# Kernel optimization log

Measured on AMD Instinct MI355X. Metric: run time of the kernel, lower is better.

## Reference

```python
import jax, jax.numpy as jnp
import numpy as np

B = 262144
INPUT_DIM = 512
HID = 64
NUM_BASE = 2
NUM_CLASSES = 2


def setup_inputs() -> dict:
    key = jax.random.key(0)
    ks = jax.random.split(key, 10)
    probs = jax.random.uniform(ks[0], (B, NUM_BASE, NUM_CLASSES), dtype=jnp.float32)
    fuzzy_features = jax.random.normal(ks[1], (B, INPUT_DIM), dtype=jnp.float32)
    s1 = 1.0 / np.sqrt(INPUT_DIM)
    s2 = 1.0 / np.sqrt(HID)
    # m1: Linear(input_dim,64) -> ReLU -> Linear(64, num_base*num_classes)
    W1 = jax.random.uniform(ks[2], (INPUT_DIM, HID), jnp.float32, -s1, s1)
    b1 = jax.random.uniform(ks[3], (HID,), jnp.float32, -s1, s1)
    W2 = jax.random.uniform(ks[4], (HID, NUM_BASE * NUM_CLASSES), jnp.float32, -s2, s2)
    b2 = jax.random.uniform(ks[5], (NUM_BASE * NUM_CLASSES,), jnp.float32, -s2, s2)
    # m2: Linear(input_dim,64) -> ReLU -> Linear(64, num_classes)
    W3 = jax.random.uniform(ks[6], (INPUT_DIM, HID), jnp.float32, -s1, s1)
    b3 = jax.random.uniform(ks[7], (HID,), jnp.float32, -s1, s1)
    W4 = jax.random.uniform(ks[8], (HID, NUM_CLASSES), jnp.float32, -s2, s2)
    b4 = jax.random.uniform(ks[9], (NUM_CLASSES,), jnp.float32, -s2, s2)
    return {"probs": probs, "fuzzy_features": fuzzy_features,
            "W1": W1, "b1": b1, "W2": W2, "b2": b2,
            "W3": W3, "b3": b3, "W4": W4, "b4": b4}


def _forward(probs, x, W1, b1, W2, b2, W3, b3, W4, b4):
    # FuzzyMeasureLearner
    h1 = jax.nn.relu(x @ W1 + b1)                       # [B, 64]
    single = jax.nn.sigmoid((h1 @ W2 + b2).reshape(-1, NUM_BASE, NUM_CLASSES))
    h2 = jax.nn.relu(x @ W3 + b3)                       # [B, 64]
    inc = jax.nn.sigmoid(h2 @ W4 + b4)                  # [B, 2]
    # Vectorized Choquet integral (binary, 2 sources)
    p0 = probs[:, 0, :]                                 # [B, 2]
    p1 = probs[:, 1, :]
    mu1 = single[:, 0, :]
    mu2 = single[:, 1, :]
    mu12 = jnp.minimum(jnp.maximum(mu1, mu2) + inc, 1.0)
    res = jnp.where(p0 <= p1,
                    p0 * mu1 + (p1 - p0) * mu12,
                    p1 * mu2 + (p0 - p1) * mu12)        # [B, 2]
    return jax.nn.softmax(res, axis=1)


def reference(probs, fuzzy_features, W1, b1, W2, b2, W3, b3, W4, b4):
    return _forward(probs, fuzzy_features, W1, b1, W2, b2, W3, b3, W4, b4)
```

## Files before the change

kernel.cpp:

```cpp
#include <hip/hip_runtime.h>
#include <hip/hip_bf16.h>

typedef short s16x8 __attribute__((ext_vector_type(8)));
typedef unsigned u32x4 __attribute__((ext_vector_type(4)));
typedef float f32x4 __attribute__((ext_vector_type(4)));
typedef float f32x2 __attribute__((ext_vector_type(2)));

static __device__ __forceinline__ short f2bf(float f) {
    unsigned u = __builtin_bit_cast(unsigned, f);
    unsigned r = (u + 0x7fffu + ((u >> 16) & 1u)) >> 16;
    return (short)r;
}

static __device__ __forceinline__ unsigned pk2bf(float a, float b) {
    __hip_bfloat162 h = __float22bfloat162_rn(make_float2(a, b));
    unsigned r;
    __builtin_memcpy(&r, &h, sizeof(r));
    return r;
}

__global__ void prep_weights(const float* __restrict__ W1,
                             const float* __restrict__ W3,
                             short* __restrict__ bws) {
    int tid = blockIdx.x * blockDim.x + threadIdx.x;
    int j  = tid & 7;
    int l  = (tid >> 3) & 63;
    int nt = (tid >> 9) & 7;
    int kk = tid >> 12;
    int k = kk * 32 + ((l >> 4) << 3) + j;
    int n = nt * 16 + (l & 15);
    float v = (n < 64) ? W1[k * 64 + n] : W3[k * 64 + (n - 64)];
    bws[tid] = f2bf(v);
}

__global__ __launch_bounds__(256, 2)
void mf2_main(const float* __restrict__ probs, const float* __restrict__ x,
              const short* __restrict__ bws,
              const float* __restrict__ b1, const float* __restrict__ W2,
              const float* __restrict__ b2, const float* __restrict__ b3,
              const float* __restrict__ W4, const float* __restrict__ b4,
              float* __restrict__ out)
{
    const int lane = threadIdx.x & 63;
    const int wv   = threadIdx.x >> 6;
    const int g    = lane >> 4;
    const int m    = lane & 15;
    const long rowBase = (long)blockIdx.x * 256 + wv * 64;

    f32x4 acc[4][8];
    #pragma unroll
    for (int t = 0; t < 4; ++t)
        #pragma unroll
        for (int nt = 0; nt < 8; ++nt)
            acc[t][nt] = (f32x4){0.f, 0.f, 0.f, 0.f};

    const float* xp = x + (rowBase + m) * 512 + g * 8;
    const s16x8* bp = (const s16x8*)bws + lane;

    f32x4 ra[4][2];
    #pragma unroll
    for (int t = 0; t < 4; ++t) {
        const float* p = xp + t * (16 * 512);
        ra[t][0] = __builtin_nontemporal_load((const f32x4*)p);
        ra[t][1] = __builtin_nontemporal_load((const f32x4*)(p + 4));
    }

    #pragma unroll 2
    for (int kk = 0; kk < 16; ++kk) {
        s16x8 b[8];
        #pragma unroll
        for (int nt = 0; nt < 8; ++nt) b[nt] = bp[kk * 512 + nt * 64];

        s16x8 a[4];
        #pragma unroll
        for (int t = 0; t < 4; ++t) {
            u32x4 pa;
            pa[0] = pk2bf(ra[t][0][0], ra[t][0][1]);
            pa[1] = pk2bf(ra[t][0][2], ra[t][0][3]);
            pa[2] = pk2bf(ra[t][1][0], ra[t][1][1]);
            pa[3] = pk2bf(ra[t][1][2], ra[t][1][3]);
            a[t] = __builtin_bit_cast(s16x8, pa);
        }

        if (kk < 15) {
            #pragma unroll
            for (int t = 0; t < 4; ++t) {
                const float* p = xp + t * (16 * 512) + (kk + 1) * 32;
                ra[t][0] = __builtin_nontemporal_load((const f32x4*)p);
                ra[t][1] = __builtin_nontemporal_load((const f32x4*)(p + 4));
            }
        }

        #pragma unroll
        for (int nt = 0; nt < 8; ++nt)
            #pragma unroll
            for (int t = 0; t < 4; ++t)
                acc[t][nt] = __builtin_amdgcn_mfma_f32_16x16x32_bf16(a[t], b[nt], acc[t][nt], 0, 0, 0);
    }

    float w2r[4][4];
    float w4r[4][2];
    float biasr[8];
    #pragma unroll
    for (int nt = 0; nt < 4; ++nt) {
        const int col = m + 16 * nt;
        f32x4 w2v = *(const f32x4*)(W2 + col * 4);
        #pragma unroll
        for (int c = 0; c < 4; ++c) w2r[nt][c] = w2v[c];
        f32x2 w4v = *(const f32x2*)(W4 + col * 2);
        w4r[nt][0] = w4v[0]; w4r[nt][1] = w4v[1];
    }
    #pragma unroll
    for (int nt = 0; nt < 8; ++nt) {
        const int col = m + 16 * nt;
        biasr[nt] = (col < 64) ? b1[col] : b3[col - 64];
    }
    float b2v[4], b4v[2];
    #pragma unroll
    for (int c = 0; c < 4; ++c) b2v[c] = b2[c];
    #pragma unroll
    for (int c = 0; c < 2; ++c) b4v[c] = b4[c];

    float own[6] = {0.f, 0.f, 0.f, 0.f, 0.f, 0.f};
    #pragma unroll
    for (int t = 0; t < 4; ++t) {
        #pragma unroll
        for (int r = 0; r < 4; ++r) {
            float v[6] = {0.f, 0.f, 0.f, 0.f, 0.f, 0.f};
            #pragma unroll
            for (int nt = 0; nt < 4; ++nt) {
                float h = fmaxf(acc[t][nt][r] + biasr[nt], 0.f);
                v[0] += h * w2r[nt][0];
                v[1] += h * w2r[nt][1];
                v[2] += h * w2r[nt][2];
                v[3] += h * w2r[nt][3];
            }
            #pragma unroll
            for (int j = 0; j < 4; ++j) {
                float h = fmaxf(acc[t][4 + j][r] + biasr[4 + j], 0.f);
                v[4] += h * w4r[j][0];
                v[5] += h * w4r[j][1];
            }
            #pragma unroll
            for (int msk = 1; msk <= 8; msk <<= 1) {
                #pragma unroll
                for (int c = 0; c < 6; ++c) v[c] += __shfl_xor(v[c], msk, 64);
            }
            if (m == t * 4 + r) {
                #pragma unroll
                for (int c = 0; c < 6; ++c) own[c] = v[c];
            }
        }
    }

    {
        const int t = m >> 2, r = m & 3;
        const long row = rowBase + t * 16 + g * 4 + r;
        f32x4 pr = *(const f32x4*)(probs + row * 4);
        float mu1[2], mu2[2], icv[2];
        #pragma unroll
        for (int c = 0; c < 2; ++c) {
            mu1[c] = 1.0f / (1.0f + __expf(-(own[c]     + b2v[c])));
            mu2[c] = 1.0f / (1.0f + __expf(-(own[2 + c] + b2v[2 + c])));
            icv[c] = 1.0f / (1.0f + __expf(-(own[4 + c] + b4v[c])));
        }
        float res[2];
        #pragma unroll
        for (int c = 0; c < 2; ++c) {
            float p0 = pr[c], p1 = pr[2 + c];
            float m12 = fminf(fmaxf(mu1[c], mu2[c]) + icv[c], 1.0f);
            res[c] = (p0 <= p1) ? (p0 * mu1[c] + (p1 - p0) * m12)
                                : (p1 * mu2[c] + (p0 - p1) * m12);
        }
        float d01 = res[0] - res[1];
        f32x2 o;
        o[0] = 1.0f / (1.0f + __expf(-d01));
        o[1] = 1.0f / (1.0f + __expf(d01));
        *(f32x2*)(out + row * 2) = o;
    }
}

extern "C" void kernel_launch(void* const* d_in, const int* in_sizes, int n_in,
                              void* d_out, int out_size, void* d_ws, size_t ws_size,
                              hipStream_t stream)
{
    const float* probs = (const float*)d_in[0];
    const float* x     = (const float*)d_in[1];
    const float* W1    = (const float*)d_in[2];
    const float* b1    = (const float*)d_in[3];
    const float* W2    = (const float*)d_in[4];
    const float* b2    = (const float*)d_in[5];
    const float* W3    = (const float*)d_in[6];
    const float* b3    = (const float*)d_in[7];
    const float* W4    = (const float*)d_in[8];
    const float* b4    = (const float*)d_in[9];
    float* out = (float*)d_out;
    short* bws = (short*)d_ws;

    hipLaunchKernelGGL(prep_weights, dim3(256), dim3(256), 0, stream, W1, W3, bws);
    hipLaunchKernelGGL(mf2_main, dim3(1024), dim3(256), 0, stream,
                       probs, x, bws, b1, W2, b2, b3, W4, b4, out);
}
```

Measured before the change: 146.4 us.

## Load 128 contiguous bytes per lane with K-permuted weights and smaller wave tiles

The packed weight layout is permuted in K so that each lane can read 32 contiguous floats (128 bytes) of x per row chunk instead of 8 scattered floats, with the MFMA k-ordering matched to the permutation. Each wave now handles 32 rows instead of 64, and the grid is doubled to 2048 blocks. The aim is wider, more coalesced global reads and more waves in flight to hide memory latency on this bandwidth-bound GEMV-like stage. The cost is more register pressure from 16 prefetched vectors per lane, and B-fragment reloads that are reused over only 2 row tiles instead of 4.

```diff
diff --git a/kernel.cpp b/kernel.cpp
--- a/kernel.cpp
+++ b/kernel.cpp
@@ -27,7 +27,8 @@
     int l  = (tid >> 3) & 63;
     int nt = (tid >> 9) & 7;
     int kk = tid >> 12;
-    int k = kk * 32 + ((l >> 4) << 3) + j;
+    int g  = l >> 4;
+    int k = ((kk >> 2) << 7) + (g << 5) + ((kk & 3) << 3) + j;
     int n = nt * 16 + (l & 15);
     float v = (n < 64) ? W1[k * 64 + n] : W3[k * 64 + (n - 64)];
     bws[tid] = f2bf(v);
@@ -45,57 +46,61 @@
     const int wv   = threadIdx.x >> 6;
     const int g    = lane >> 4;
     const int m    = lane & 15;
-    const long rowBase = (long)blockIdx.x * 256 + wv * 64;
-
-    f32x4 acc[4][8];
-    #pragma unroll
-    for (int t = 0; t < 4; ++t)
+    const long rowBase = (long)blockIdx.x * 128 + wv * 32;
+
+    f32x4 acc[2][8];
+    #pragma unroll
+    for (int t = 0; t < 2; ++t)
         #pragma unroll
         for (int nt = 0; nt < 8; ++nt)
             acc[t][nt] = (f32x4){0.f, 0.f, 0.f, 0.f};
 
-    const float* xp = x + (rowBase + m) * 512 + g * 8;
+    const float* xp = x + (rowBase + m) * 512 + g * 32;
     const s16x8* bp = (const s16x8*)bws + lane;
 
-    f32x4 ra[4][2];
-    #pragma unroll
-    for (int t = 0; t < 4; ++t) {
-        const float* p = xp + t * (16 * 512);
-        ra[t][0] = __builtin_nontemporal_load((const f32x4*)p);
-        ra[t][1] = __builtin_nontemporal_load((const f32x4*)(p + 4));
-    }
-
-    #pragma unroll 2
-    for (int kk = 0; kk < 16; ++kk) {
-        s16x8 b[8];
-        #pragma unroll
-        for (int nt = 0; nt < 8; ++nt) b[nt] = bp[kk * 512 + nt * 64];
-
-        s16x8 a[4];
-        #pragma unroll
-        for (int t = 0; t < 4; ++t) {
-            u32x4 pa;
-            pa[0] = pk2bf(ra[t][0][0], ra[t][0][1]);
-            pa[1] = pk2bf(ra[t][0][2], ra[t][0][3]);
-            pa[2] = pk2bf(ra[t][1][0], ra[t][1][1]);
-            pa[3] = pk2bf(ra[t][1][2], ra[t][1][3]);
-            a[t] = __builtin_bit_cast(s16x8, pa);
-        }
-
-        if (kk < 15) {
-            #pragma unroll
-            for (int t = 0; t < 4; ++t) {
-                const float* p = xp + t * (16 * 512) + (kk + 1) * 32;
-                ra[t][0] = __builtin_nontemporal_load((const f32x4*)p);
-                ra[t][1] = __builtin_nontemporal_load((const f32x4*)(p + 4));
-            }
-        }
-
-        #pragma unroll
-        for (int nt = 0; nt < 8; ++nt)
-            #pragma unroll
-            for (int t = 0; t < 4; ++t)
-                acc[t][nt] = __builtin_amdgcn_mfma_f32_16x16x32_bf16(a[t], b[nt], acc[t][nt], 0, 0, 0);
+    f32x4 ra[2][8];
+    #pragma unroll
+    for (int t = 0; t < 2; ++t)
+        #pragma unroll
+        for (int q = 0; q < 8; ++q)
+            ra[t][q] = __builtin_nontemporal_load((const f32x4*)(xp + t * (16 * 512)) + q);
+
+    #pragma unroll
+    for (int c = 0; c < 4; ++c) {
+        s16x8 a[2][4];
+        #pragma unroll
+        for (int t = 0; t < 2; ++t)
+            #pragma unroll
+            for (int s = 0; s < 4; ++s) {
+                u32x4 pa;
+                pa[0] = pk2bf(ra[t][2 * s][0],     ra[t][2 * s][1]);
+                pa[1] = pk2bf(ra[t][2 * s][2],     ra[t][2 * s][3]);
+                pa[2] = pk2bf(ra[t][2 * s + 1][0], ra[t][2 * s + 1][1]);
+                pa[3] = pk2bf(ra[t][2 * s + 1][2], ra[t][2 * s + 1][3]);
+                a[t][s] = __builtin_bit_cast(s16x8, pa);
+            }
+
+        if (c < 3) {
+            #pragma unroll
+            for (int t = 0; t < 2; ++t)
+                #pragma unroll
+                for (int q = 0; q < 8; ++q)
+                    ra[t][q] = __builtin_nontemporal_load(
+                        (const f32x4*)(xp + t * (16 * 512) + (c + 1) * 128) + q);
+        }
+
+        #pragma unroll
+        for (int s = 0; s < 4; ++s) {
+            const int kk = c * 4 + s;
+            s16x8 b[8];
+            #pragma unroll
+            for (int nt = 0; nt < 8; ++nt) b[nt] = bp[kk * 512 + nt * 64];
+            #pragma unroll
+            for (int nt = 0; nt < 8; ++nt)
+                #pragma unroll
+                for (int t = 0; t < 2; ++t)
+                    acc[t][nt] = __builtin_amdgcn_mfma_f32_16x16x32_bf16(a[t][s], b[nt], acc[t][nt], 0, 0, 0);
+        }
     }
 
     float w2r[4][4];
@@ -123,7 +128,7 @@
 
     float own[6] = {0.f, 0.f, 0.f, 0.f, 0.f, 0.f};
     #pragma unroll
-    for (int t = 0; t < 4; ++t) {
+    for (int t = 0; t < 2; ++t) {
         #pragma unroll
         for (int r = 0; r < 4; ++r) {
             float v[6] = {0.f, 0.f, 0.f, 0.f, 0.f, 0.f};
@@ -153,7 +158,7 @@
         }
     }
 
-    {
+    if (m < 8) {
         const int t = m >> 2, r = m & 3;
         const long row = rowBase + t * 16 + g * 4 + r;
         f32x4 pr = *(const f32x4*)(probs + row * 4);
@@ -198,6 +203,6 @@
     short* bws = (short*)d_ws;
 
     hipLaunchKernelGGL(prep_weights, dim3(256), dim3(256), 0, stream, W1, W3, bws);
-    hipLaunchKernelGGL(mf2_main, dim3(1024), dim3(256), 0, stream,
+    hipLaunchKernelGGL(mf2_main, dim3(2048), dim3(256), 0, stream,
                        probs, x, bws, b1, W2, b2, b3, W4, b4, out);
 }
```

Result: slower. 476.5 us (+225.4%).
